# Performance work log

Hardware: AMD Instinct MI355X
Metric: run time of the kernel (lower is better)

## Reference

```python
import jax, jax.numpy as jnp
import numpy as np

HIDDEN = 256
GROUPS = 4
GDIM = HIDDEN // GROUPS  # 64


def setup_inputs() -> dict:
    key = jax.random.key(0)
    k1, k2, k3, k4 = jax.random.split(key, 4)
    B, N, P = 8, 300, 32
    x = jax.random.normal(k1, (B, N, P, HIDDEN), dtype=jnp.float32)
    query_content = jax.random.normal(k2, (B, N, HIDDEN), dtype=jnp.float32)
    out_dim = GDIM * GDIM * GROUPS
    # nn.Linear default init: U(-1/sqrt(fan_in), 1/sqrt(fan_in))
    bound = 1.0 / np.sqrt(HIDDEN)
    W_gen = jax.random.uniform(k3, (HIDDEN, out_dim), dtype=jnp.float32, minval=-bound, maxval=bound)
    b_gen = jax.random.uniform(k4, (out_dim,), dtype=jnp.float32, minval=-bound, maxval=bound)
    gamma = jnp.ones((HIDDEN,), dtype=jnp.float32)
    beta = jnp.zeros((HIDDEN,), dtype=jnp.float32)
    return {"x": x, "query_content": query_content, "W_gen": W_gen, "b_gen": b_gen, "gamma": gamma, "beta": beta}


def _layer_norm(h, gamma, beta, eps=1e-5):
    mu = jnp.mean(h, axis=-1, keepdims=True)
    var = jnp.var(h, axis=-1, keepdims=True)
    return (h - mu) * jax.lax.rsqrt(var + eps) * gamma + beta


def reference(x, query_content, W_gen, b_gen, gamma, beta):
    B, N, P, C = x.shape
    # dynamic per-query weights: [B,N,G,gd,gd]
    w = (query_content @ W_gen + b_gen).reshape(B, N, GROUPS, GDIM, GDIM)
    xg = x.reshape(B, N, P, GROUPS, GDIM)
    # mixed[...,p,g,e] = sum_d xg[...,p,g,d] * w[...,g,e,d]  (matmul with W^T)
    mixed = jnp.einsum('bnpgd,bnged->bnpge', xg, w).reshape(B, N, P, C)
    return jax.nn.relu(_layer_norm(mixed, gamma, beta))
```

## Files before the change

### kernel.cpp

```cpp
#include <hip/hip_runtime.h>
#include <hip/hip_bf16.h>

typedef __attribute__((ext_vector_type(4))) float floatx4;
typedef __attribute__((ext_vector_type(8))) short short8;

#define HIDDEN 256
#define NOUT 16384

__device__ __forceinline__ short bf16bits(float x) {
    __hip_bfloat16 h = __float2bfloat16(x);
    return __builtin_bit_cast(short, h);
}

__global__ __launch_bounds__(256) void kA_gemm_w(
    const float* __restrict__ qc, const float* __restrict__ Wg,
    const float* __restrict__ bg, __hip_bfloat16* __restrict__ wdyn, int M)
{
    __shared__ short As[64 * 40];
    __shared__ short Bs[64 * 40];

    const int tid  = threadIdx.x;
    const int wave = tid >> 6, lane = tid & 63;
    const int lq   = lane & 15, quad = lane >> 4;
    const int n0   = blockIdx.x * 64;
    const int m0   = blockIdx.y * 64;

    floatx4 acc[4];
    #pragma unroll
    for (int t = 0; t < 4; ++t) acc[t] = (floatx4){0.f, 0.f, 0.f, 0.f};

    const int ar = tid >> 2;
    const int ac = (tid & 3) << 3;
    const int gm_a = m0 + ar;
    const int bn = tid & 63;
    const int bk = (tid >> 6) << 3;

    for (int k0 = 0; k0 < HIDDEN; k0 += 32) {
        float4 f0 = make_float4(0.f,0.f,0.f,0.f), f1 = make_float4(0.f,0.f,0.f,0.f);
        if (gm_a < M) {
            const float4* s = reinterpret_cast<const float4*>(qc + (size_t)gm_a * HIDDEN + k0 + ac);
            f0 = s[0]; f1 = s[1];
        }
        short8 av;
        av[0]=bf16bits(f0.x); av[1]=bf16bits(f0.y); av[2]=bf16bits(f0.z); av[3]=bf16bits(f0.w);
        av[4]=bf16bits(f1.x); av[5]=bf16bits(f1.y); av[6]=bf16bits(f1.z); av[7]=bf16bits(f1.w);
        *reinterpret_cast<short8*>(&As[ar*40 + ac]) = av;

        {
            const float* bsrc = Wg + (size_t)(k0 + bk) * NOUT + n0 + bn;
            short8 bv;
            #pragma unroll
            for (int j = 0; j < 8; ++j) bv[j] = bf16bits(bsrc[(size_t)j * NOUT]);
            *reinterpret_cast<short8*>(&Bs[bn*40 + bk]) = bv;
        }
        __syncthreads();

        short8 a = *reinterpret_cast<const short8*>(&As[(wave*16 + lq)*40 + quad*8]);
        #pragma unroll
        for (int t = 0; t < 4; ++t) {
            short8 b = *reinterpret_cast<const short8*>(&Bs[(t*16 + lq)*40 + quad*8]);
            acc[t] = __builtin_amdgcn_mfma_f32_16x16x32_bf16(a, b, acc[t], 0, 0, 0);
        }
        __syncthreads();
    }

    #pragma unroll
    for (int t = 0; t < 4; ++t) {
        const int gn = n0 + t*16 + lq;
        const float bv = bg[gn];
        #pragma unroll
        for (int r = 0; r < 4; ++r) {
            const int gm = m0 + wave*16 + quad*4 + r;
            if (gm < M) wdyn[(size_t)gm * NOUT + gn] = __float2bfloat16(acc[t][r] + bv);
        }
    }
}

__global__ __launch_bounds__(256) void kB_mix_ln(
    const float* __restrict__ x, const __hip_bfloat16* __restrict__ wdyn,
    const float* __restrict__ gamma, const float* __restrict__ beta,
    float* __restrict__ out)
{
    __shared__ short xs[32 * 264];
    __shared__ short ws2[256 * 72];
    __shared__ float ms[32 * 260];
    __shared__ float gs[256], bs2[256];

    const int tid  = threadIdx.x;
    const int bnq  = blockIdx.x;
    const int wave = tid >> 6, lane = tid & 63;
    const int lq   = lane & 15, quad = lane >> 4;

    gs[tid]  = gamma[tid];
    bs2[tid] = beta[tid];

    {
        const float4* xg = reinterpret_cast<const float4*>(x + (size_t)bnq * (32 * 256));
        #pragma unroll
        for (int i = 0; i < 4; ++i) {
            const int idx8 = tid + 256 * i;
            const float4 f0 = xg[idx8*2], f1 = xg[idx8*2 + 1];
            const int lin = idx8 * 8;
            const int p = lin >> 8, c = lin & 255;
            short8 v;
            v[0]=bf16bits(f0.x); v[1]=bf16bits(f0.y); v[2]=bf16bits(f0.z); v[3]=bf16bits(f0.w);
            v[4]=bf16bits(f1.x); v[5]=bf16bits(f1.y); v[6]=bf16bits(f1.z); v[7]=bf16bits(f1.w);
            *reinterpret_cast<short8*>(&xs[p*264 + c]) = v;
        }
    }
    {
        const uint4* wg = reinterpret_cast<const uint4*>(wdyn + (size_t)bnq * NOUT);
        #pragma unroll
        for (int i = 0; i < 8; ++i) {
            const int q = tid + 256 * i;
            const uint4 v = wg[q];
            const int j = q * 8;
            const int co = j >> 6, d = j & 63;
            *reinterpret_cast<uint4*>(&ws2[co*72 + d]) = v;
        }
    }
    __syncthreads();

    const int mtile = wave & 1;
    floatx4 acc[2][4];
    #pragma unroll
    for (int gi = 0; gi < 2; ++gi)
        #pragma unroll
        for (int nt = 0; nt < 4; ++nt) acc[gi][nt] = (floatx4){0.f, 0.f, 0.f, 0.f};

    #pragma unroll
    for (int gi = 0; gi < 2; ++gi) {
        const int g = (wave >> 1) * 2 + gi;
        #pragma unroll
        for (int ks = 0; ks < 2; ++ks) {
            short8 a = *reinterpret_cast<const short8*>(&xs[(mtile*16 + lq)*264 + g*64 + ks*32 + quad*8]);
            #pragma unroll
            for (int nt = 0; nt < 4; ++nt) {
                short8 b = *reinterpret_cast<const short8*>(&ws2[(g*64 + nt*16 + lq)*72 + ks*32 + quad*8]);
                acc[gi][nt] = __builtin_amdgcn_mfma_f32_16x16x32_bf16(a, b, acc[gi][nt], 0, 0, 0);
            }
        }
    }

    #pragma unroll
    for (int gi = 0; gi < 2; ++gi) {
        const int g = (wave >> 1) * 2 + gi;
        #pragma unroll
        for (int nt = 0; nt < 4; ++nt) {
            const int c = g*64 + nt*16 + lq;
            #pragma unroll
            for (int r = 0; r < 4; ++r) {
                const int p = mtile*16 + quad*4 + r;
                ms[p*260 + c] = acc[gi][nt][r];
            }
        }
    }
    __syncthreads();

    const int p = tid >> 3, ch = tid & 7;
    const float* row = &ms[p*260 + ch*32];
    float v[32];
    float s = 0.f, ss = 0.f;
    #pragma unroll
    for (int i = 0; i < 8; ++i) {
        const float4 q = reinterpret_cast<const float4*>(row)[i];
        v[i*4+0]=q.x; v[i*4+1]=q.y; v[i*4+2]=q.z; v[i*4+3]=q.w;
        s  += q.x + q.y + q.z + q.w;
        ss += q.x*q.x + q.y*q.y + q.z*q.z + q.w*q.w;
    }
    #pragma unroll
    for (int off = 1; off < 8; off <<= 1) {
        s  += __shfl_xor(s,  off);
        ss += __shfl_xor(ss, off);
    }
    const float mu = s * (1.f/256.f);
    float var = ss * (1.f/256.f) - mu*mu;
    var = fmaxf(var, 0.f);
    const float rs = rsqrtf(var + 1e-5f);

    float* orow = out + (size_t)bnq * (32*256) + p*256 + ch*32;
    #pragma unroll
    for (int i = 0; i < 8; ++i) {
        const int c = ch*32 + i*4;
        float4 q;
        q.x = fmaxf((v[i*4+0]-mu)*rs*gs[c+0] + bs2[c+0], 0.f);
        q.y = fmaxf((v[i*4+1]-mu)*rs*gs[c+1] + bs2[c+1], 0.f);
        q.z = fmaxf((v[i*4+2]-mu)*rs*gs[c+2] + bs2[c+2], 0.f);
        q.w = fmaxf((v[i*4+3]-mu)*rs*gs[c+3] + bs2[c+3], 0.f);
        reinterpret_cast<float4*>(orow)[i] = q;
    }
}

extern "C" void kernel_launch(void* const* d_in, const int* in_sizes, int n_in,
                              void* d_out, int out_size, void* d_ws, size_t ws_size,
                              hipStream_t stream)
{
    const float* x     = (const float*)d_in[0];
    const float* qc    = (const float*)d_in[1];
    const float* Wg    = (const float*)d_in[2];
    const float* bg    = (const float*)d_in[3];
    const float* gamma = (const float*)d_in[4];
    const float* beta  = (const float*)d_in[5];
    float* out = (float*)d_out;
    __hip_bfloat16* wdyn = (__hip_bfloat16*)d_ws;

    const int M = in_sizes[1] / HIDDEN;

    dim3 gA(NOUT / 64, (M + 63) / 64);
    kA_gemm_w<<<gA, 256, 0, stream>>>(qc, Wg, bg, wdyn, M);
    kB_mix_ln<<<M, 256, 0, stream>>>(x, wdyn, gamma, beta, out);
}
```

Baseline: 267.0 us.

## Pre-convert inputs to bf16, retile weight GEMM to 128x128, fuse LN in registers

Adds two pre-pass kernels: one converts query_content to bf16, the other transposes W_gen into a bf16 K-contiguous layout. The dynamic-weight GEMM then uses 128x128 tiles with 4x4 MFMA fragments per wave and direct global-to-LDS loads with a swizzled layout, replacing the strided per-element fp32 loads. The mixing kernel drops most LDS staging: it reads x and the dynamic weights straight into MFMA fragments and computes LayerNorm statistics from the accumulators with shuffles plus a small cross-wave reduction. The cost is extra launches and workspace traffic for the converted copies, plus scattered scalar output stores.

```diff
diff --git a/kernel.cpp b/kernel.cpp
--- a/kernel.cpp
+++ b/kernel.cpp
@@ -12,182 +12,237 @@
     return __builtin_bit_cast(short, h);
 }
 
-__global__ __launch_bounds__(256) void kA_gemm_w(
-    const float* __restrict__ qc, const float* __restrict__ Wg,
-    const float* __restrict__ bg, __hip_bfloat16* __restrict__ wdyn, int M)
-{
-    __shared__ short As[64 * 40];
-    __shared__ short Bs[64 * 40];
+#define GLDS16(gsrc, ldst) \
+    __builtin_amdgcn_global_load_lds((const __attribute__((address_space(1))) void*)(gsrc), \
+                                     (__attribute__((address_space(3))) void*)(ldst), 16, 0, 0)
+
+__global__ __launch_bounds__(256) void kC(const float* __restrict__ src, short* __restrict__ dst, int n4)
+{
+    int i = blockIdx.x * 256 + threadIdx.x;
+    if (i >= n4) return;
+    float4 f = reinterpret_cast<const float4*>(src)[i];
+    short4 v;
+    v.x = bf16bits(f.x); v.y = bf16bits(f.y); v.z = bf16bits(f.z); v.w = bf16bits(f.w);
+    reinterpret_cast<short4*>(dst)[i] = v;
+}
+
+__global__ __launch_bounds__(256) void kT(const float* __restrict__ Wg, short* __restrict__ WgT)
+{
+    __shared__ short t[64 * 68];
+    const int tid = threadIdx.x;
+    const int n0 = blockIdx.x * 64, k0 = blockIdx.y * 64;
+
+    const int r  = tid >> 4;
+    const int c4 = tid & 15;
+    #pragma unroll
+    for (int i = 0; i < 4; ++i) {
+        const int kl = r + i * 16;
+        float4 f = *reinterpret_cast<const float4*>(Wg + (size_t)(k0 + kl) * NOUT + n0 + c4 * 4);
+        short4 v;
+        v.x = bf16bits(f.x); v.y = bf16bits(f.y); v.z = bf16bits(f.z); v.w = bf16bits(f.w);
+        *reinterpret_cast<short4*>(&t[kl * 68 + c4 * 4]) = v;
+    }
+    __syncthreads();
+
+    #pragma unroll
+    for (int h = 0; h < 2; ++h) {
+        const int id = tid + h * 256;
+        const int nl = id >> 3, kc = id & 7;
+        short8 v;
+        #pragma unroll
+        for (int j = 0; j < 8; ++j) v[j] = t[(kc * 8 + j) * 68 + nl];
+        *reinterpret_cast<short8*>(WgT + (size_t)(n0 + nl) * HIDDEN + k0 + kc * 8) = v;
+    }
+}
+
+__global__ __launch_bounds__(256) void kA2(
+    const short* __restrict__ qcb, const short* __restrict__ WgT,
+    const float* __restrict__ bg, short* __restrict__ wdyn, int M)
+{
+    __shared__ short As[128 * 32];
+    __shared__ short Bs[128 * 32];
 
     const int tid  = threadIdx.x;
     const int wave = tid >> 6, lane = tid & 63;
     const int lq   = lane & 15, quad = lane >> 4;
-    const int n0   = blockIdx.x * 64;
-    const int m0   = blockIdx.y * 64;
-
-    floatx4 acc[4];
-    #pragma unroll
-    for (int t = 0; t < 4; ++t) acc[t] = (floatx4){0.f, 0.f, 0.f, 0.f};
-
-    const int ar = tid >> 2;
-    const int ac = (tid & 3) << 3;
-    const int gm_a = m0 + ar;
-    const int bn = tid & 63;
-    const int bk = (tid >> 6) << 3;
+    const int wm   = wave >> 1, wn = wave & 1;
+    const int m0   = blockIdx.y * 128;
+    const int n0   = blockIdx.x * 128;
+
+    const int ml = lane >> 2;
+    const int kq = (lane & 3) ^ ((lane >> 3) & 3);
+
+    int rowA0 = m0 + wave * 32 + ml;       if (rowA0 >= M) rowA0 = M - 1;
+    int rowA1 = m0 + wave * 32 + 16 + ml;  if (rowA1 >= M) rowA1 = M - 1;
+    const int rowB0 = n0 + wave * 32 + ml;
+    const int rowB1 = rowB0 + 16;
+    const short* aSrc0 = qcb + (size_t)rowA0 * HIDDEN + kq * 8;
+    const short* aSrc1 = qcb + (size_t)rowA1 * HIDDEN + kq * 8;
+    const short* bSrc0 = WgT + (size_t)rowB0 * HIDDEN + kq * 8;
+    const short* bSrc1 = WgT + (size_t)rowB1 * HIDDEN + kq * 8;
+    short* aDst0 = &As[(wave * 32) * 32];
+    short* aDst1 = &As[(wave * 32 + 16) * 32];
+    short* bDst0 = &Bs[(wave * 32) * 32];
+    short* bDst1 = &Bs[(wave * 32 + 16) * 32];
+
+    const int kswz = quad ^ ((lq >> 1) & 3);
+    const short* aFrag[4];
+    const short* bFrag[4];
+    #pragma unroll
+    for (int i = 0; i < 4; ++i) {
+        aFrag[i] = &As[(wm * 64 + i * 16 + lq) * 32 + kswz * 8];
+        bFrag[i] = &Bs[(wn * 64 + i * 16 + lq) * 32 + kswz * 8];
+    }
+
+    floatx4 acc[4][4];
+    #pragma unroll
+    for (int i = 0; i < 4; ++i)
+        #pragma unroll
+        for (int j = 0; j < 4; ++j) acc[i][j] = (floatx4){0.f, 0.f, 0.f, 0.f};
 
     for (int k0 = 0; k0 < HIDDEN; k0 += 32) {
-        float4 f0 = make_float4(0.f,0.f,0.f,0.f), f1 = make_float4(0.f,0.f,0.f,0.f);
-        if (gm_a < M) {
-            const float4* s = reinterpret_cast<const float4*>(qc + (size_t)gm_a * HIDDEN + k0 + ac);
-            f0 = s[0]; f1 = s[1];
-        }
-        short8 av;
-        av[0]=bf16bits(f0.x); av[1]=bf16bits(f0.y); av[2]=bf16bits(f0.z); av[3]=bf16bits(f0.w);
-        av[4]=bf16bits(f1.x); av[5]=bf16bits(f1.y); av[6]=bf16bits(f1.z); av[7]=bf16bits(f1.w);
-        *reinterpret_cast<short8*>(&As[ar*40 + ac]) = av;
-
-        {
-            const float* bsrc = Wg + (size_t)(k0 + bk) * NOUT + n0 + bn;
-            short8 bv;
-            #pragma unroll
-            for (int j = 0; j < 8; ++j) bv[j] = bf16bits(bsrc[(size_t)j * NOUT]);
-            *reinterpret_cast<short8*>(&Bs[bn*40 + bk]) = bv;
-        }
+        GLDS16(aSrc0, aDst0);
+        GLDS16(aSrc1, aDst1);
+        GLDS16(bSrc0, bDst0);
+        GLDS16(bSrc1, bDst1);
+        aSrc0 += 32; aSrc1 += 32; bSrc0 += 32; bSrc1 += 32;
         __syncthreads();
 
-        short8 a = *reinterpret_cast<const short8*>(&As[(wave*16 + lq)*40 + quad*8]);
-        #pragma unroll
-        for (int t = 0; t < 4; ++t) {
-            short8 b = *reinterpret_cast<const short8*>(&Bs[(t*16 + lq)*40 + quad*8]);
-            acc[t] = __builtin_amdgcn_mfma_f32_16x16x32_bf16(a, b, acc[t], 0, 0, 0);
-        }
+        short8 a[4], b[4];
+        #pragma unroll
+        for (int i = 0; i < 4; ++i) a[i] = *reinterpret_cast<const short8*>(aFrag[i]);
+        #pragma unroll
+        for (int j = 0; j < 4; ++j) b[j] = *reinterpret_cast<const short8*>(bFrag[j]);
+        #pragma unroll
+        for (int i = 0; i < 4; ++i)
+            #pragma unroll
+            for (int j = 0; j < 4; ++j)
+                acc[i][j] = __builtin_amdgcn_mfma_f32_16x16x32_bf16(a[i], b[j], acc[i][j], 0, 0, 0);
         __syncthreads();
     }
 
     #pragma unroll
-    for (int t = 0; t < 4; ++t) {
-        const int gn = n0 + t*16 + lq;
-        const float bv = bg[gn];
-        #pragma unroll
-        for (int r = 0; r < 4; ++r) {
-            const int gm = m0 + wave*16 + quad*4 + r;
-            if (gm < M) wdyn[(size_t)gm * NOUT + gn] = __float2bfloat16(acc[t][r] + bv);
-        }
-    }
-}
-
-__global__ __launch_bounds__(256) void kB_mix_ln(
-    const float* __restrict__ x, const __hip_bfloat16* __restrict__ wdyn,
+    for (int j = 0; j < 4; ++j) {
+        const int col = n0 + wn * 64 + j * 16 + lq;
+        const float bv = bg[col];
+        #pragma unroll
+        for (int i = 0; i < 4; ++i) {
+            const int rbase = m0 + wm * 64 + i * 16 + quad * 4;
+            #pragma unroll
+            for (int r = 0; r < 4; ++r) {
+                const int row = rbase + r;
+                if (row < M) wdyn[(size_t)row * NOUT + col] = bf16bits(acc[i][j][r] + bv);
+            }
+        }
+    }
+}
+
+__global__ __launch_bounds__(256) void kB2(
+    const float* __restrict__ x, const short* __restrict__ wdyn,
     const float* __restrict__ gamma, const float* __restrict__ beta,
     float* __restrict__ out)
 {
-    __shared__ short xs[32 * 264];
-    __shared__ short ws2[256 * 72];
-    __shared__ float ms[32 * 260];
-    __shared__ float gs[256], bs2[256];
+    __shared__ float red[2][4][4][2][2];
 
     const int tid  = threadIdx.x;
     const int bnq  = blockIdx.x;
     const int wave = tid >> 6, lane = tid & 63;
     const int lq   = lane & 15, quad = lane >> 4;
-
-    gs[tid]  = gamma[tid];
-    bs2[tid] = beta[tid];
-
-    {
-        const float4* xg = reinterpret_cast<const float4*>(x + (size_t)bnq * (32 * 256));
-        #pragma unroll
-        for (int i = 0; i < 4; ++i) {
-            const int idx8 = tid + 256 * i;
-            const float4 f0 = xg[idx8*2], f1 = xg[idx8*2 + 1];
-            const int lin = idx8 * 8;
-            const int p = lin >> 8, c = lin & 255;
+    const int mtile = wave & 1, gp = wave >> 1;
+
+    const float* xr = x + (size_t)bnq * (32 * HIDDEN) + (mtile * 16 + lq) * HIDDEN;
+    const short* wr = wdyn + (size_t)bnq * NOUT;
+
+    short8 afr[2][2];
+    #pragma unroll
+    for (int gi = 0; gi < 2; ++gi) {
+        const int g = gp * 2 + gi;
+        #pragma unroll
+        for (int ks = 0; ks < 2; ++ks) {
+            const float4* s = reinterpret_cast<const float4*>(xr + g * 64 + ks * 32 + quad * 8);
+            const float4 f0 = s[0], f1 = s[1];
             short8 v;
             v[0]=bf16bits(f0.x); v[1]=bf16bits(f0.y); v[2]=bf16bits(f0.z); v[3]=bf16bits(f0.w);
             v[4]=bf16bits(f1.x); v[5]=bf16bits(f1.y); v[6]=bf16bits(f1.z); v[7]=bf16bits(f1.w);
-            *reinterpret_cast<short8*>(&xs[p*264 + c]) = v;
-        }
-    }
-    {
-        const uint4* wg = reinterpret_cast<const uint4*>(wdyn + (size_t)bnq * NOUT);
-        #pragma unroll
-        for (int i = 0; i < 8; ++i) {
-            const int q = tid + 256 * i;
-            const uint4 v = wg[q];
-            const int j = q * 8;
-            const int co = j >> 6, d = j & 63;
-            *reinterpret_cast<uint4*>(&ws2[co*72 + d]) = v;
+            afr[gi][ks] = v;
+        }
+    }
+
+    floatx4 acc[2][4];
+    #pragma unroll
+    for (int gi = 0; gi < 2; ++gi)
+        #pragma unroll
+        for (int nt = 0; nt < 4; ++nt) acc[gi][nt] = (floatx4){0.f, 0.f, 0.f, 0.f};
+
+    #pragma unroll
+    for (int gi = 0; gi < 2; ++gi) {
+        const int g = gp * 2 + gi;
+        #pragma unroll
+        for (int ks = 0; ks < 2; ++ks) {
+            #pragma unroll
+            for (int nt = 0; nt < 4; ++nt) {
+                const short8 b = *reinterpret_cast<const short8*>(
+                    wr + (g * 64 + nt * 16 + lq) * 64 + ks * 32 + quad * 8);
+                acc[gi][nt] = __builtin_amdgcn_mfma_f32_16x16x32_bf16(afr[gi][ks], b, acc[gi][nt], 0, 0, 0);
+            }
+        }
+    }
+
+    float s[4], ss[4];
+    #pragma unroll
+    for (int r = 0; r < 4; ++r) { s[r] = 0.f; ss[r] = 0.f; }
+    #pragma unroll
+    for (int gi = 0; gi < 2; ++gi)
+        #pragma unroll
+        for (int nt = 0; nt < 4; ++nt)
+            #pragma unroll
+            for (int r = 0; r < 4; ++r) {
+                const float v = acc[gi][nt][r];
+                s[r] += v; ss[r] += v * v;
+            }
+    #pragma unroll
+    for (int off = 1; off < 16; off <<= 1) {
+        #pragma unroll
+        for (int r = 0; r < 4; ++r) {
+            s[r]  += __shfl_xor(s[r],  off);
+            ss[r] += __shfl_xor(ss[r], off);
+        }
+    }
+    if (lq == 0) {
+        #pragma unroll
+        for (int r = 0; r < 4; ++r) {
+            red[mtile][quad][r][gp][0] = s[r];
+            red[mtile][quad][r][gp][1] = ss[r];
         }
     }
     __syncthreads();
 
-    const int mtile = wave & 1;
-    floatx4 acc[2][4];
-    #pragma unroll
-    for (int gi = 0; gi < 2; ++gi)
-        #pragma unroll
-        for (int nt = 0; nt < 4; ++nt) acc[gi][nt] = (floatx4){0.f, 0.f, 0.f, 0.f};
-
+    float mu[4], rs[4];
+    #pragma unroll
+    for (int r = 0; r < 4; ++r) {
+        const float S  = s[r]  + red[mtile][quad][r][gp ^ 1][0];
+        const float SS = ss[r] + red[mtile][quad][r][gp ^ 1][1];
+        mu[r] = S * (1.f / 256.f);
+        float var = SS * (1.f / 256.f) - mu[r] * mu[r];
+        var = fmaxf(var, 0.f);
+        rs[r] = rsqrtf(var + 1e-5f);
+    }
+
+    float* orow = out + (size_t)bnq * (32 * HIDDEN);
     #pragma unroll
     for (int gi = 0; gi < 2; ++gi) {
-        const int g = (wave >> 1) * 2 + gi;
-        #pragma unroll
-        for (int ks = 0; ks < 2; ++ks) {
-            short8 a = *reinterpret_cast<const short8*>(&xs[(mtile*16 + lq)*264 + g*64 + ks*32 + quad*8]);
-            #pragma unroll
-            for (int nt = 0; nt < 4; ++nt) {
-                short8 b = *reinterpret_cast<const short8*>(&ws2[(g*64 + nt*16 + lq)*72 + ks*32 + quad*8]);
-                acc[gi][nt] = __builtin_amdgcn_mfma_f32_16x16x32_bf16(a, b, acc[gi][nt], 0, 0, 0);
-            }
-        }
-    }
-
-    #pragma unroll
-    for (int gi = 0; gi < 2; ++gi) {
-        const int g = (wave >> 1) * 2 + gi;
+        const int g = gp * 2 + gi;
         #pragma unroll
         for (int nt = 0; nt < 4; ++nt) {
-            const int c = g*64 + nt*16 + lq;
+            const int c = g * 64 + nt * 16 + lq;
+            const float gm = gamma[c], bt = beta[c];
             #pragma unroll
             for (int r = 0; r < 4; ++r) {
-                const int p = mtile*16 + quad*4 + r;
-                ms[p*260 + c] = acc[gi][nt][r];
-            }
-        }
-    }
-    __syncthreads();
-
-    const int p = tid >> 3, ch = tid & 7;
-    const float* row = &ms[p*260 + ch*32];
-    float v[32];
-    float s = 0.f, ss = 0.f;
-    #pragma unroll
-    for (int i = 0; i < 8; ++i) {
-        const float4 q = reinterpret_cast<const float4*>(row)[i];
-        v[i*4+0]=q.x; v[i*4+1]=q.y; v[i*4+2]=q.z; v[i*4+3]=q.w;
-        s  += q.x + q.y + q.z + q.w;
-        ss += q.x*q.x + q.y*q.y + q.z*q.z + q.w*q.w;
-    }
-    #pragma unroll
-    for (int off = 1; off < 8; off <<= 1) {
-        s  += __shfl_xor(s,  off);
-        ss += __shfl_xor(ss, off);
-    }
-    const float mu = s * (1.f/256.f);
-    float var = ss * (1.f/256.f) - mu*mu;
-    var = fmaxf(var, 0.f);
-    const float rs = rsqrtf(var + 1e-5f);
-
-    float* orow = out + (size_t)bnq * (32*256) + p*256 + ch*32;
-    #pragma unroll
-    for (int i = 0; i < 8; ++i) {
-        const int c = ch*32 + i*4;
-        float4 q;
-        q.x = fmaxf((v[i*4+0]-mu)*rs*gs[c+0] + bs2[c+0], 0.f);
-        q.y = fmaxf((v[i*4+1]-mu)*rs*gs[c+1] + bs2[c+1], 0.f);
-        q.z = fmaxf((v[i*4+2]-mu)*rs*gs[c+2] + bs2[c+2], 0.f);
-        q.w = fmaxf((v[i*4+3]-mu)*rs*gs[c+3] + bs2[c+3], 0.f);
-        reinterpret_cast<float4*>(orow)[i] = q;
+                const int p = mtile * 16 + quad * 4 + r;
+                const float v = fmaxf((acc[gi][nt][r] - mu[r]) * rs[r] * gm + bt, 0.f);
+                orow[p * HIDDEN + c] = v;
+            }
+        }
     }
 }
 
@@ -202,11 +257,19 @@
     const float* gamma = (const float*)d_in[4];
     const float* beta  = (const float*)d_in[5];
     float* out = (float*)d_out;
-    __hip_bfloat16* wdyn = (__hip_bfloat16*)d_ws;
 
     const int M = in_sizes[1] / HIDDEN;
 
-    dim3 gA(NOUT / 64, (M + 63) / 64);
-    kA_gemm_w<<<gA, 256, 0, stream>>>(qc, Wg, bg, wdyn, M);
-    kB_mix_ln<<<M, 256, 0, stream>>>(x, wdyn, gamma, beta, out);
-}
+    char* ws = (char*)d_ws;
+    short* wdyn = (short*)ws;
+    short* WgT  = (short*)(ws + (size_t)M * NOUT * 2);
+    short* qcb  = (short*)(ws + (size_t)M * NOUT * 2 + (size_t)NOUT * HIDDEN * 2);
+
+    {
+        const int n4 = (M * HIDDEN) / 4;
+        kC<<<(n4 + 255) / 256, 256, 0, stream>>>(qc, qcb, n4);
+    }
+    kT<<<dim3(NOUT / 64, HIDDEN / 64), 256, 0, stream>>>(Wg, WgT);
+    kA2<<<dim3(NOUT / 128, (M + 127) / 128), 256, 0, stream>>>(qcb, WgT, bg, wdyn, M);
+    kB2<<<M, 256, 0, stream>>>(x, wdyn, gamma, beta, out);
+}
```

After: 252.3 us. 5.5% less time.
